# Kernel tuning notes

Measured on AMD Instinct MI355X. Metric: run time of the kernel, lower is better.

Reference implementation:

```python
import jax, jax.numpy as jnp
import numpy as np

B, T, N, CIN = 64, 24, 256, 1  # batch, n_his, n stations, in channels
F1, F2, OUTC = 64, 128, 1      # blocks [[64,64],[64,128]], output channels
K = 3                          # conv kernel size


def conv2d_same(x, w):  # x [B,H,W,C], w [K,K,C,O]
    return jax.lax.conv_general_dilated(x, w, (1, 1), 'SAME',
                                        dimension_numbers=('NHWC', 'HWIO', 'NHWC'))


def conv1d_same(x, w):  # x [B,N,C], w [K,C,O]
    return jax.lax.conv_general_dilated(x, w, (1,), 'SAME',
                                        dimension_numbers=('NWC', 'WIO', 'NWC'))


def hard_sigmoid(x):  # keras ConvLSTM default recurrent_activation
    return jnp.clip(x * 0.2 + 0.5, 0.0, 1.0)


def l2_normalize_23(x):  # tf.nn.l2_normalize over axes [2,3]
    sq = jnp.sum(x * x, axis=(2, 3), keepdims=True)
    return x * jax.lax.rsqrt(jnp.maximum(sq, 1e-12))


def convlstm1d(x_seq, kx, kh, b, return_sequences):
    # x_seq [B,T,N,C]; kx [K,C,4F]; kh [K,F,4F]; b [4F]
    Bs, Ts, Ns, Cs = x_seq.shape
    F = kh.shape[1]
    # input convolutions are time-independent: do them all at once
    xg = conv1d_same(x_seq.reshape(Bs * Ts, Ns, Cs), kx).reshape(Bs, Ts, Ns, 4 * F) + b
    xg = jnp.moveaxis(xg, 1, 0)  # [T,B,N,4F]
    h0 = jnp.zeros((Bs, Ns, F), x_seq.dtype)
    c0 = jnp.zeros((Bs, Ns, F), x_seq.dtype)

    def step(carry, xt):
        h, c = carry
        g = xt + conv1d_same(h, kh)                 # [B,N,4F]
        gi, gf, gc, go = jnp.split(g, 4, axis=-1)
        i = hard_sigmoid(gi)
        f = hard_sigmoid(gf)
        o = hard_sigmoid(go)
        c = f * c + i * jnp.tanh(gc)
        h = o * jnp.tanh(c)
        return (h, c), (h if return_sequences else jnp.zeros((), x_seq.dtype))

    (hT, _), hs = jax.lax.scan(step, (h0, c0), xg)
    if return_sequences:
        return jnp.moveaxis(hs, 0, 1)  # [B,T,N,F]
    return hT                          # [B,N,F]


def setup_inputs() -> dict:
    key = jax.random.key(0)
    ks = jax.random.split(key, 14)
    s = 0.1
    return {
        'x': jax.random.normal(ks[0], (B, T, N, CIN), jnp.float32),
        'conv1_w': jax.random.normal(ks[1], (K, K, CIN, F1), jnp.float32) * s,
        'conv1_b': jnp.zeros((F1,), jnp.float32),
        'conv2_w': jax.random.normal(ks[2], (K, K, F1, F1), jnp.float32) * s,
        'conv2_b': jnp.zeros((F1,), jnp.float32),
        'kx1': jax.random.normal(ks[3], (K, F1, 4 * F1), jnp.float32) * s,
        'kh1': jax.random.normal(ks[4], (K, F1, 4 * F1), jnp.float32) * s,
        'b1': jnp.zeros((4 * F1,), jnp.float32),
        'kx2': jax.random.normal(ks[5], (K, F1, 4 * F2), jnp.float32) * s,
        'kh2': jax.random.normal(ks[6], (K, F2, 4 * F2), jnp.float32) * s,
        'b2': jnp.zeros((4 * F2,), jnp.float32),
        'fc_w': jax.random.normal(ks[7], (F2, OUTC), jnp.float32) * s,
        'fc_b': jnp.zeros((OUTC,), jnp.float32),
    }


def reference(x, conv1_w, conv1_b, conv2_w, conv2_b, kx1, kh1, b1,
              kx2, kh2, b2, fc_w, fc_b):
    # spatial conv stack (Conv2D 3x3 same, linear activation)
    h = conv2d_same(x, conv1_w) + conv1_b
    h = conv2d_same(h, conv2_w) + conv2_b
    # dropout = identity at inference; norm == 'L2'
    h = l2_normalize_23(h)
    # stacked ConvLSTM1D: return_sequences=True then False
    h = convlstm1d(h, kx1, kh1, b1, True)    # [B,T,N,F1]
    h = convlstm1d(h, kx2, kh2, b2, False)   # [B,N,F2]
    h = h[:, None]                            # reshape (-1, 1, N, F2)
    h = l2_normalize_23(h)
    # FullyConLayer: 1x1 FC over channels -> outc
    y = jnp.einsum('bunc,co->buno', h, fc_w) + fc_b
    return y.reshape(-1, 1, N, OUTC)
```

## Files before the change

### kernel.cpp

```cpp
#include <hip/hip_runtime.h>
#include <hip/hip_bf16.h>

using bf16 = __hip_bfloat16;
typedef unsigned short u16;
typedef unsigned int u32;
typedef __attribute__((ext_vector_type(8))) short short8;
typedef __attribute__((ext_vector_type(4))) float floatx4;

#define DEVI __device__ __forceinline__

constexpr int B = 64, T = 24, N = 256, F1 = 64, F2 = 128;
constexpr int GG = 8;

DEVI float b2f(bf16 v) { return __bfloat162float(v); }
DEVI float b2fu(u16 u) { return __uint_as_float(((u32)u) << 16); }
DEVI u16 f2b(float f) {
    u32 u = __float_as_uint(f);
    u32 r = (u + 0x7FFF + ((u >> 16) & 1)) >> 16;
    return (u16)r;
}
DEVI float hsig(float x) { x = x * 0.2f + 0.5f; return fminf(fmaxf(x, 0.f), 1.f); }

#if __has_builtin(__builtin_amdgcn_global_load_lds)
#define ASYNC16(gsrc, ldst)                                                            \
    __builtin_amdgcn_global_load_lds((const __attribute__((address_space(1))) u32*)(gsrc), \
                                     (__attribute__((address_space(3))) u32*)(ldst), 16, 0, 0)
#define HAVE_ASYNC 1
#else
#define HAVE_ASYNC 0
#endif

DEVI float read_in(const void* p, long i, int isbf) {
    return isbf ? b2f(((const bf16*)p)[i]) : ((const float*)p)[i];
}

__global__ void init_flag(int* flag) { *flag = 1; }
__global__ void detect_scan(const u16* __restrict__ xu, int* __restrict__ flag) {
    int i0 = blockIdx.x * 2048 + threadIdx.x;
    int hit = 0;
    for (int i = i0; i < (blockIdx.x + 1) * 2048; i += 256)
        if (((xu[i] >> 7) & 0xFF) == 0xFF) hit = 1;
    if (hit) *flag = 0;
}

struct CvtDesc { const void* src; float* dst; int n; };
struct CvtPack { CvtDesc d[8]; };
__global__ void cvt_pack(CvtPack p, const int* __restrict__ flag) {
    CvtDesc c = p.d[blockIdx.x];
    int isbf = *flag;
    for (int i = threadIdx.x; i < c.n; i += 256)
        c.dst[i] = c.src ? read_in(c.src, i, isbf) : 0.f;
}

__global__ void repack_w(const void* __restrict__ kxr, const void* __restrict__ khr,
                         u16* __restrict__ Wt, int CIN, int F, const int* __restrict__ flag) {
    int NG = 4 * F, CH = CIN + F, K = 3 * CH;
    int idx = blockIdx.x * 256 + threadIdx.x;
    if (idx >= NG * K) return;
    int g = idx / K, k = idx - g * K;
    int kn = k / CH, c = k - kn * CH;
    int isbf = *flag;
    float v = (c < CIN) ? read_in(kxr, (long)(kn * CIN + c) * NG + g, isbf)
                        : read_in(khr, (long)(kn * F + (c - CIN)) * NG + g, isbf);
    Wt[(long)g * K + k] = f2b(v);
}

__global__ void repack_w2(const void* __restrict__ w2r, u16* __restrict__ w2b,
                          const int* __restrict__ flag) {
    int idx = blockIdx.x * 256 + threadIdx.x;
    if (idx >= 64 * 576) return;
    int f = idx / 576, k = idx - f * 576;
    int kt = k / 192, rem = k - kt * 192, kn = rem >> 6, c = rem & 63;
    float v = read_in(w2r, (long)((kt * 3 + kn) * 64 + c) * 64 + f, *flag);
    w2b[(long)f * 576 + k] = f2b(v);
}

__global__ __launch_bounds__(256)
void conv1_grp(const void* __restrict__ xraw, const float* __restrict__ w1c,
               const float* __restrict__ b1v, u16* __restrict__ c1grp,
               const int* __restrict__ flag, int g0) {
    __shared__ float sxw[3 * 260];
    int s = blockIdx.x, b = blockIdx.y, tid = threadIdx.x;
    int tt = g0 * GG - 1 + s;
    u16* dst = c1grp + ((long)s * B + b) * N * 64;
    if (tt < 0 || tt >= T) {
        for (int i = tid; i < N * 64 / 4; i += 256) *(uint2*)&dst[i * 4] = uint2{0, 0};
        return;
    }
    int isbf = *flag;
    for (int i = tid; i < 3 * 258; i += 256) {
        int r = i / 258, cc = i - r * 258;
        int ttt = tt - 1 + r, nn = cc - 1;
        float v = 0.f;
        if (ttt >= 0 && ttt < T && nn >= 0 && nn < N)
            v = read_in(xraw, (long)(b * T + ttt) * N + nn, isbf);
        sxw[r * 260 + cc] = v;
    }
    __syncthreads();
    int c = tid & 63, ngq = tid >> 6;
    float w[9];
#pragma unroll
    for (int j = 0; j < 9; j++) w[j] = w1c[j * 64 + c];
    float bias = b1v[c];
    for (int j = 0; j < 64; j++) {
        int n = ngq * 64 + j;
        float v = bias;
#pragma unroll
        for (int dt = 0; dt < 3; dt++)
#pragma unroll
            for (int dn = 0; dn < 3; dn++)
                v += sxw[dt * 260 + n + dn] * w[dt * 3 + dn];
        dst[n * 64 + c] = f2b(v);
    }
}

__global__ __launch_bounds__(256)
void conv_mfma(const u16* __restrict__ c1grp, const u16* __restrict__ w2b,
               const float* __restrict__ b2v, u16* __restrict__ xs8,
               float* __restrict__ ssq, int g0) {
    constexpr int CP1 = 72;
    __shared__ __align__(16) u16 win1[3 * 66 * CP1];
    __shared__ __align__(16) u16 bch[2 * 2048];
    __shared__ float red[256];

    int tid = threadIdx.x;
    int bb = blockIdx.y, n0 = blockIdx.x * 64, z = blockIdx.z;
    int t = g0 * GG + z;
    int w = tid >> 6, l15 = tid & 15, q = (tid >> 4) & 3;

    for (int i = tid; i < 3 * 66 * 8; i += 256) {
        int u = i & 7, rr = i >> 3;
        int kt = rr / 66, r1 = rr - kt * 66;
        int nn = n0 - 1 + r1;
        uint4 v{0, 0, 0, 0};
        if (nn >= 0 && nn < N)
            v = *(const uint4*)&c1grp[((((long)(z + kt)) * B + bb) * N + nn) * 64 + u * 8];
        *(uint4*)&win1[(kt * 66 + r1) * CP1 + u * 8] = v;
    }

    auto stage = [&](int kk, int bufi) {
        int g = tid >> 2, u = tid & 3;
        int k = kk * 32 + ((u ^ (g & 3)) << 3);
#if HAVE_ASYNC
        ASYNC16(w2b + (long)g * 576 + k, &bch[bufi * 2048 + tid * 8]);
#else
        uint4 v = *(const uint4*)(w2b + (long)g * 576 + k);
        *(uint4*)&bch[bufi * 2048 + tid * 8] = v;
#endif
    };
    stage(0, 0);
    __syncthreads();

    floatx4 acc[4] = {};
    for (int kk = 0; kk < 18; ++kk) {
        int cur = kk & 1;
        if (kk + 1 < 18) stage(kk + 1, 1 - cur);
        int kbase = kk * 32;
        int kt = kbase / 192, rem = kbase - kt * 192, kn = rem >> 6, c0 = rem & 63;
        int gcol = w * 16 + l15;
        short8 bf = *(const short8*)&bch[cur * 2048 + gcol * 32 + ((q ^ (gcol & 3)) << 3)];
#pragma unroll
        for (int mi = 0; mi < 4; mi++) {
            short8 af = *(const short8*)&win1[(kt * 66 + mi * 16 + l15 + kn) * CP1 + c0 + q * 8];
            acc[mi] = __builtin_amdgcn_mfma_f32_16x16x32_bf16(af, bf, acc[mi], 0, 0, 0);
        }
        __syncthreads();
    }

    u16* xslice = xs8 + (long)z * B * N * 64;
    int f = w * 16 + l15;
    float bias2 = b2v[f];
    float lsum = 0.f;
#pragma unroll
    for (int mi = 0; mi < 4; mi++)
#pragma unroll
        for (int r = 0; r < 4; r++) {
            int n = n0 + mi * 16 + q * 4 + r;
            float v = acc[mi][r] + bias2;
            lsum += v * v;
            xslice[((long)bb * N + n) * 64 + f] = f2b(v);
        }
    red[tid] = lsum; __syncthreads();
    for (int k = 128; k > 0; k >>= 1) {
        if (tid < k) red[tid] += red[tid + k];
        __syncthreads();
    }
    if (tid == 0) atomicAdd(&ssq[bb * T + t], red[0]);
}

template<int CIN, int F, int FL>
__global__ __launch_bounds__(512, 4)
void lstm_mfma(const u16* __restrict__ xin, const u16* __restrict__ hprev,
               u16* __restrict__ hnext, float* __restrict__ cst,
               const u16* __restrict__ Wt, const float* __restrict__ bias,
               const float* __restrict__ ssqp, int t) {
    constexpr int CH = CIN + F;
    constexpr int CHP = CH + 8;
    constexpr int K = 3 * CH;
    constexpr int NK = K / 32;
    constexpr int NGL = 4 * FL;
    constexpr int NGP = NGL + 4;
    constexpr int NI = NGL / 128;
    constexpr int BCH = NGL * 32;
    constexpr int GLD_USH = 32 * NGP * 2;
    constexpr int UNION_USH = (2 * BCH > GLD_USH) ? 2 * BCH : GLD_USH;
    constexpr int LOGFL = (FL == 64) ? 6 : 5;

    __shared__ __align__(16) u16 win[66 * CHP];
    __shared__ __align__(16) u16 ubuf[UNION_USH];
    u16* bch = ubuf;
    float* Gld = (float*)ubuf;

    int tid = threadIdx.x;
    int bb = blockIdx.y, n0 = blockIdx.x * 64, z = blockIdx.z;
    int w = tid >> 6, l15 = tid & 15, q = (tid >> 4) & 3;

    float scale = 1.f;
    if (ssqp) scale = rsqrtf(fmaxf(ssqp[bb * T + t], 1e-12f));

    constexpr int GRP = CH / 4;
    for (int i = tid; i < 66 * GRP; i += 512) {
        int row = i / GRP, g4 = (i - row * GRP) * 4;
        int n = n0 + row - 1;
        uint2 v{};
        if (n >= 0 && n < N) {
            if (g4 < CIN) {
                v = *(const uint2*)&xin[((long)bb * N + n) * CIN + g4];
                if (ssqp) {
                    u16 e0 = f2b(b2fu((u16)(v.x & 0xFFFF)) * scale);
                    u16 e1 = f2b(b2fu((u16)(v.x >> 16)) * scale);
                    u16 e2 = f2b(b2fu((u16)(v.y & 0xFFFF)) * scale);
                    u16 e3 = f2b(b2fu((u16)(v.y >> 16)) * scale);
                    v.x = (u32)e0 | ((u32)e1 << 16);
                    v.y = (u32)e2 | ((u32)e3 << 16);
                }
            } else if (t > 0) {
                v = *(const uint2*)&hprev[((long)bb * N + n) * F + (g4 - CIN)];
            }
        }
        *(uint2*)&win[row * CHP + g4] = v;
    }

    auto stage = [&](int kk, int bufi) {
#pragma unroll
        for (int it = 0; it < NGL / 128; ++it) {
            int P = it * 512 + tid;
            int r = P >> 2, u = P & 3;
            int gt = r >> LOGFL, fl = r & (FL - 1);
            long g = (long)gt * F + z * FL + fl;
            int k = kk * 32 + ((u ^ (r & 3)) << 3);
#if HAVE_ASYNC
            ASYNC16(Wt + g * K + k, &bch[bufi * BCH + P * 8]);
#else
            uint4 v = *(const uint4*)(Wt + g * K + k);
            *(uint4*)&bch[bufi * BCH + P * 8] = v;
#endif
        }
    };
    stage(0, 0);
    __syncthreads();

    floatx4 acc[4][NI] = {};
    for (int kk = 0; kk < NK; ++kk) {
        int cur = kk & 1;
        if (kk + 1 < NK) stage(kk + 1, 1 - cur);
        int kbase = kk * 32;
        int kn = kbase / CH, c0 = kbase - kn * CH;
        short8 af[4];
#pragma unroll
        for (int mi = 0; mi < 4; mi++)
            af[mi] = *(const short8*)&win[(mi * 16 + l15 + kn) * CHP + c0 + q * 8];
#pragma unroll
        for (int ni = 0; ni < NI; ni++) {
            int r = w * (NI * 16) + ni * 16 + l15;
            short8 bf = *(const short8*)&bch[cur * BCH + r * 32 + ((q ^ (r & 3)) << 3)];
#pragma unroll
            for (int mi = 0; mi < 4; mi++)
                acc[mi][ni] = __builtin_amdgcn_mfma_f32_16x16x32_bf16(af[mi], bf, acc[mi][ni], 0, 0, 0);
        }
        __syncthreads();
    }

    for (int h = 0; h < 2; ++h) {
#pragma unroll
        for (int mi2 = 0; mi2 < 2; ++mi2) {
            int mi = h * 2 + mi2;
#pragma unroll
            for (int ni = 0; ni < NI; ni++)
#pragma unroll
                for (int r = 0; r < 4; r++)
                    Gld[(mi2 * 16 + q * 4 + r) * NGP + w * (NI * 16) + ni * 16 + l15] = acc[mi][ni][r];
        }
        __syncthreads();
        for (int i = tid; i < 32 * FL; i += 512) {
            int m = i >> LOGFL, fl = i & (FL - 1);
            int fz = z * FL + fl;
            float gi = Gld[m * NGP + fl]          + bias[fz];
            float gf = Gld[m * NGP + FL + fl]     + bias[F + fz];
            float gc = Gld[m * NGP + 2 * FL + fl] + bias[2 * F + fz];
            float go = Gld[m * NGP + 3 * FL + fl] + bias[3 * F + fz];
            int n = n0 + h * 32 + m;
            long ci = ((long)bb * N + n) * F + fz;
            float cp = (t > 0) ? cst[ci] : 0.f;
            float iv = hsig(gi), fv = hsig(gf), ov = hsig(go);
            float cn = fv * cp + iv * tanhf(gc);
            cst[ci] = cn;
            hnext[ci] = f2b(ov * tanhf(cn));
        }
        __syncthreads();
    }
}

__global__ void final_kernel(const u16* __restrict__ hT, const float* __restrict__ fcw,
                             const float* __restrict__ fcb, void* __restrict__ out,
                             const int* __restrict__ flag) {
    __shared__ float red[256];
    int b = blockIdx.x, tid = threadIdx.x;
    const u16* hb = hT + (long)b * N * 128;
    float s = 0.f;
    for (int i = tid; i < N * 128; i += 256) { float v = b2fu(hb[i]); s += v * v; }
    red[tid] = s; __syncthreads();
    for (int k = 128; k > 0; k >>= 1) {
        if (tid < k) red[tid] += red[tid + k];
        __syncthreads();
    }
    float scale = rsqrtf(fmaxf(red[0], 1e-12f));
    int n = tid;
    float acc = fcb[0];
    for (int c = 0; c < 128; c++) acc += b2fu(hb[n * 128 + c]) * scale * fcw[c];
    if (*flag) ((bf16*)out)[b * N + n] = __float2bfloat16(acc);
    else       ((float*)out)[b * N + n] = acc;
}

extern "C" void kernel_launch(void* const* d_in, const int* in_sizes, int n_in,
                              void* d_out, int out_size, void* d_ws, size_t ws_size,
                              hipStream_t stream) {
    float* ws = (float*)d_ws;
    u16* xs8    = (u16*)ws;
    u16* c1grp  = (u16*)(ws + 4194304);
    u16* h1A    = (u16*)(ws + 9437184);
    u16* h1B    = (u16*)(ws + 9961472);
    u16* h2A    = (u16*)(ws + 10485760);
    u16* h2B    = (u16*)(ws + 11534336);
    float* c1   = ws + 12582912;
    float* c2   = ws + 13631488;
    u16* Wt1    = (u16*)(ws + 15728640);
    u16* Wt2    = (u16*)(ws + 15777792);
    u16* w2b    = (u16*)(ws + 15925248);
    float* w1c  = ws + 15943680;
    float* bb1  = ws + 15944256;
    float* bb2  = ws + 15944320;
    float* bg1  = ws + 15944384;
    float* bg2  = ws + 15944640;
    float* fcwf = ws + 15945152;
    float* fcbf = ws + 15945280;
    float* ssq  = ws + 15945281;
    int*   flag = (int*)(ws + 15946817);

    init_flag<<<1, 1, 0, stream>>>(flag);
    detect_scan<<<32, 256, 0, stream>>>((const u16*)d_in[0], flag);

    CvtPack pk;
    pk.d[0] = {d_in[1],  w1c,  576};
    pk.d[1] = {d_in[2],  bb1,  64};
    pk.d[2] = {d_in[4],  bb2,  64};
    pk.d[3] = {d_in[7],  bg1,  256};
    pk.d[4] = {d_in[10], bg2,  512};
    pk.d[5] = {d_in[11], fcwf, 128};
    pk.d[6] = {d_in[12], fcbf, 1};
    pk.d[7] = {nullptr,  ssq,  B * T};
    cvt_pack<<<8, 256, 0, stream>>>(pk, flag);

    repack_w<<<(256 * 384 + 255) / 256, 256, 0, stream>>>(d_in[5], d_in[6], Wt1, 64, 64, flag);
    repack_w<<<(512 * 576 + 255) / 256, 256, 0, stream>>>(d_in[8], d_in[9], Wt2, 64, 128, flag);
    repack_w2<<<(64 * 576 + 255) / 256, 256, 0, stream>>>(d_in[3], w2b, flag);

    for (int g = 0; g < T / GG; g++) {
        conv1_grp<<<dim3(GG + 2, B), 256, 0, stream>>>(d_in[0], w1c, bb1, c1grp, flag, g);
        conv_mfma<<<dim3(4, B, GG), 256, 0, stream>>>(c1grp, w2b, bb2, xs8, ssq, g);
        for (int ti = 0; ti < GG; ti++) {
            int t = g * GG + ti;
            const u16* h1p = (t & 1) ? h1A : h1B;
            u16* h1n = (t & 1) ? h1B : h1A;
            lstm_mfma<64, 64, 32><<<dim3(4, B, 2), 512, 0, stream>>>(
                xs8 + (long)ti * B * N * 64, h1p, h1n, c1, Wt1, bg1, ssq, t);
            const u16* h2p = (t & 1) ? h2A : h2B;
            u16* h2n = (t & 1) ? h2B : h2A;
            lstm_mfma<64, 128, 64><<<dim3(4, B, 2), 512, 0, stream>>>(
                h1n, h2p, h2n, c2, Wt2, bg2, nullptr, t);
        }
    }
    final_kernel<<<B, 256, 0, stream>>>(h2B, fcwf, fcbf, d_out, flag);
}
```

Before: 997.8 us.

## Wavefront-pipeline both LSTM layers in one launch and precompute convs for all steps

Measured after the change: 1.933 ms. 1.94x slower.

```diff
diff --git a/kernel.cpp b/kernel.cpp
--- a/kernel.cpp
+++ b/kernel.cpp
@@ -10,7 +10,6 @@
 #define DEVI __device__ __forceinline__
 
 constexpr int B = 64, T = 24, N = 256, F1 = 64, F2 = 128;
-constexpr int GG = 8;
 
 DEVI float b2f(bf16 v) { return __bfloat162float(v); }
 DEVI float b2fu(u16 u) { return __uint_as_float(((u32)u) << 16); }
@@ -76,13 +75,13 @@
 }
 
 __global__ __launch_bounds__(256)
-void conv1_grp(const void* __restrict__ xraw, const float* __restrict__ w1c,
-               const float* __restrict__ b1v, u16* __restrict__ c1grp,
-               const int* __restrict__ flag, int g0) {
+void conv1_all(const void* __restrict__ xraw, const float* __restrict__ w1c,
+               const float* __restrict__ b1v, u16* __restrict__ c1all,
+               const int* __restrict__ flag) {
     __shared__ float sxw[3 * 260];
     int s = blockIdx.x, b = blockIdx.y, tid = threadIdx.x;
-    int tt = g0 * GG - 1 + s;
-    u16* dst = c1grp + ((long)s * B + b) * N * 64;
+    int tt = s - 1;
+    u16* dst = c1all + ((long)s * B + b) * N * 64;
     if (tt < 0 || tt >= T) {
         for (int i = tid; i < N * 64 / 4; i += 256) *(uint2*)&dst[i * 4] = uint2{0, 0};
         return;
@@ -115,17 +114,16 @@
 }
 
 __global__ __launch_bounds__(256)
-void conv_mfma(const u16* __restrict__ c1grp, const u16* __restrict__ w2b,
-               const float* __restrict__ b2v, u16* __restrict__ xs8,
-               float* __restrict__ ssq, int g0) {
+void conv_mfma(const u16* __restrict__ c1all, const u16* __restrict__ w2b,
+               const float* __restrict__ b2v, u16* __restrict__ xs24,
+               float* __restrict__ ssq) {
     constexpr int CP1 = 72;
     __shared__ __align__(16) u16 win1[3 * 66 * CP1];
     __shared__ __align__(16) u16 bch[2 * 2048];
     __shared__ float red[256];
 
     int tid = threadIdx.x;
-    int bb = blockIdx.y, n0 = blockIdx.x * 64, z = blockIdx.z;
-    int t = g0 * GG + z;
+    int bb = blockIdx.y, n0 = blockIdx.x * 64, t = blockIdx.z;
     int w = tid >> 6, l15 = tid & 15, q = (tid >> 4) & 3;
 
     for (int i = tid; i < 3 * 66 * 8; i += 256) {
@@ -134,7 +132,7 @@
         int nn = n0 - 1 + r1;
         uint4 v{0, 0, 0, 0};
         if (nn >= 0 && nn < N)
-            v = *(const uint4*)&c1grp[((((long)(z + kt)) * B + bb) * N + nn) * 64 + u * 8];
+            v = *(const uint4*)&c1all[((((long)(t + kt)) * B + bb) * N + nn) * 64 + u * 8];
         *(uint4*)&win1[(kt * 66 + r1) * CP1 + u * 8] = v;
     }
 
@@ -167,7 +165,7 @@
         __syncthreads();
     }
 
-    u16* xslice = xs8 + (long)z * B * N * 64;
+    u16* xslice = xs24 + (long)t * B * N * 64;
     int f = w * 16 + l15;
     float bias2 = b2v[f];
     float lsum = 0.f;
@@ -189,11 +187,12 @@
 }
 
 template<int CIN, int F, int FL>
-__global__ __launch_bounds__(512, 4)
-void lstm_mfma(const u16* __restrict__ xin, const u16* __restrict__ hprev,
-               u16* __restrict__ hnext, float* __restrict__ cst,
-               const u16* __restrict__ Wt, const float* __restrict__ bias,
-               const float* __restrict__ ssqp, int t) {
+DEVI void lstm_unit(u16* win, u16* ubuf,
+                    const u16* __restrict__ xin, const u16* __restrict__ hprev,
+                    u16* __restrict__ hnext, float* __restrict__ cst,
+                    const u16* __restrict__ Wt, const float* __restrict__ bias,
+                    const float* __restrict__ ssqp, int t,
+                    int bx, int by, int bz, int tid) {
     constexpr int CH = CIN + F;
     constexpr int CHP = CH + 8;
     constexpr int K = 3 * CH;
@@ -202,17 +201,12 @@
     constexpr int NGP = NGL + 4;
     constexpr int NI = NGL / 128;
     constexpr int BCH = NGL * 32;
-    constexpr int GLD_USH = 32 * NGP * 2;
-    constexpr int UNION_USH = (2 * BCH > GLD_USH) ? 2 * BCH : GLD_USH;
     constexpr int LOGFL = (FL == 64) ? 6 : 5;
 
-    __shared__ __align__(16) u16 win[66 * CHP];
-    __shared__ __align__(16) u16 ubuf[UNION_USH];
     u16* bch = ubuf;
     float* Gld = (float*)ubuf;
 
-    int tid = threadIdx.x;
-    int bb = blockIdx.y, n0 = blockIdx.x * 64, z = blockIdx.z;
+    int bb = by, n0 = bx * 64, z = bz;
     int w = tid >> 6, l15 = tid & 15, q = (tid >> 4) & 3;
 
     float scale = 1.f;
@@ -311,6 +305,27 @@
     }
 }
 
+__global__ __launch_bounds__(512, 4)
+void lstm_pair(const u16* __restrict__ x1, const u16* __restrict__ h1p, u16* __restrict__ h1n,
+               float* __restrict__ c1, const u16* __restrict__ Wt1, const float* __restrict__ bg1,
+               const float* __restrict__ ssq,
+               const u16* __restrict__ h1c2, const u16* __restrict__ h2p, u16* __restrict__ h2n,
+               float* __restrict__ c2, const u16* __restrict__ Wt2, const float* __restrict__ bg2,
+               int p) {
+    __shared__ __align__(16) u16 win[66 * 200];
+    __shared__ __align__(16) u16 ubuf[16640];
+    int z = blockIdx.z, tid = threadIdx.x;
+    if (z == 0) {
+        if (p >= T) return;
+        lstm_unit<64, 64, 64>(win, ubuf, x1, h1p, h1n, c1, Wt1, bg1, ssq, p,
+                              blockIdx.x, blockIdx.y, 0, tid);
+    } else {
+        if (p < 1) return;
+        lstm_unit<64, 128, 64>(win, ubuf, h1c2, h2p, h2n, c2, Wt2, bg2, nullptr, p - 1,
+                               blockIdx.x, blockIdx.y, z - 1, tid);
+    }
+}
+
 __global__ void final_kernel(const u16* __restrict__ hT, const float* __restrict__ fcw,
                              const float* __restrict__ fcb, void* __restrict__ out,
                              const int* __restrict__ flag) {
@@ -336,26 +351,26 @@
                               void* d_out, int out_size, void* d_ws, size_t ws_size,
                               hipStream_t stream) {
     float* ws = (float*)d_ws;
-    u16* xs8    = (u16*)ws;
-    u16* c1grp  = (u16*)(ws + 4194304);
-    u16* h1A    = (u16*)(ws + 9437184);
-    u16* h1B    = (u16*)(ws + 9961472);
-    u16* h2A    = (u16*)(ws + 10485760);
-    u16* h2B    = (u16*)(ws + 11534336);
-    float* c1   = ws + 12582912;
-    float* c2   = ws + 13631488;
-    u16* Wt1    = (u16*)(ws + 15728640);
-    u16* Wt2    = (u16*)(ws + 15777792);
-    u16* w2b    = (u16*)(ws + 15925248);
-    float* w1c  = ws + 15943680;
-    float* bb1  = ws + 15944256;
-    float* bb2  = ws + 15944320;
-    float* bg1  = ws + 15944384;
-    float* bg2  = ws + 15944640;
-    float* fcwf = ws + 15945152;
-    float* fcbf = ws + 15945280;
-    float* ssq  = ws + 15945281;
-    int*   flag = (int*)(ws + 15946817);
+    u16* xs24   = (u16*)ws;
+    u16* c1all  = (u16*)(ws + 12582912);
+    u16* h1A    = (u16*)(ws + 26214400);
+    u16* h1B    = (u16*)(ws + 26738688);
+    u16* h2A    = (u16*)(ws + 27262976);
+    u16* h2B    = (u16*)(ws + 28311552);
+    float* c1   = ws + 29360128;
+    float* c2   = ws + 30408704;
+    u16* Wt1    = (u16*)(ws + 32505856);
+    u16* Wt2    = (u16*)(ws + 32555008);
+    u16* w2b    = (u16*)(ws + 32702464);
+    float* w1c  = ws + 32720896;
+    float* bb1  = ws + 32721472;
+    float* bb2  = ws + 32721536;
+    float* bg1  = ws + 32721600;
+    float* bg2  = ws + 32721856;
+    float* fcwf = ws + 32722368;
+    float* fcbf = ws + 32722496;
+    float* ssq  = ws + 32722497;
+    int*   flag = (int*)(ws + 32724033);
 
     init_flag<<<1, 1, 0, stream>>>(flag);
     detect_scan<<<32, 256, 0, stream>>>((const u16*)d_in[0], flag);
@@ -375,20 +390,20 @@
     repack_w<<<(512 * 576 + 255) / 256, 256, 0, stream>>>(d_in[8], d_in[9], Wt2, 64, 128, flag);
     repack_w2<<<(64 * 576 + 255) / 256, 256, 0, stream>>>(d_in[3], w2b, flag);
 
-    for (int g = 0; g < T / GG; g++) {
-        conv1_grp<<<dim3(GG + 2, B), 256, 0, stream>>>(d_in[0], w1c, bb1, c1grp, flag, g);
-        conv_mfma<<<dim3(4, B, GG), 256, 0, stream>>>(c1grp, w2b, bb2, xs8, ssq, g);
-        for (int ti = 0; ti < GG; ti++) {
-            int t = g * GG + ti;
-            const u16* h1p = (t & 1) ? h1A : h1B;
-            u16* h1n = (t & 1) ? h1B : h1A;
-            lstm_mfma<64, 64, 32><<<dim3(4, B, 2), 512, 0, stream>>>(
-                xs8 + (long)ti * B * N * 64, h1p, h1n, c1, Wt1, bg1, ssq, t);
-            const u16* h2p = (t & 1) ? h2A : h2B;
-            u16* h2n = (t & 1) ? h2B : h2A;
-            lstm_mfma<64, 128, 64><<<dim3(4, B, 2), 512, 0, stream>>>(
-                h1n, h2p, h2n, c2, Wt2, bg2, nullptr, t);
-        }
+    conv1_all<<<dim3(26, B), 256, 0, stream>>>(d_in[0], w1c, bb1, c1all, flag);
+    conv_mfma<<<dim3(4, B, 24), 256, 0, stream>>>(c1all, w2b, bb2, xs24, ssq);
+
+    for (int p = 0; p <= T; p++) {
+        int t1 = p, t2 = p - 1;
+        const u16* h1p = (t1 & 1) ? h1A : h1B;
+        u16* h1n = (t1 & 1) ? h1B : h1A;
+        const u16* x1 = xs24 + (long)((t1 < T) ? t1 : 0) * B * N * 64;
+        const u16* h1c2 = (t2 & 1) ? h1B : h1A;
+        const u16* h2p = (t2 & 1) ? h2A : h2B;
+        u16* h2n = (t2 & 1) ? h2B : h2A;
+        lstm_pair<<<dim3(4, B, 3), 512, 0, stream>>>(
+            x1, h1p, h1n, c1, Wt1, bg1, ssq,
+            h1c2, h2p, h2n, c2, Wt2, bg2, p);
     }
     final_kernel<<<B, 256, 0, stream>>>(h2B, fcwf, fcbf, d_out, flag);
 }
```
